# Kernel tuning notes

Hardware: AMD Instinct MI355X
Metric: run time of the kernel (lower is better)

The kernel has to match this reference:

```python
import jax, jax.numpy as jnp
import numpy as np

EPS = 1e-12  # torch F.normalize default eps


def l2_normalize_c(x):
    # F.normalize over channel dim (dim=1): x / max(||x||_2, eps)
    nrm = jnp.sqrt(jnp.sum(x * x, axis=1, keepdims=True))
    return x / jnp.maximum(nrm, EPS)


def resize_bilinear_ac(x, H, W):
    # bilinear, align_corners=True (matches torch F.interpolate)
    n, c, h, w = x.shape
    ys = jnp.linspace(0.0, h - 1.0, H)
    xs = jnp.linspace(0.0, w - 1.0, W)
    y0 = jnp.floor(ys).astype(jnp.int32)
    y1 = jnp.minimum(y0 + 1, h - 1)
    wy = (ys - y0.astype(ys.dtype))[:, None]          # [H,1]
    x0 = jnp.floor(xs).astype(jnp.int32)
    x1 = jnp.minimum(x0 + 1, w - 1)
    wx = xs - x0.astype(xs.dtype)                      # [W]
    rows = x[:, :, y0, :] * (1.0 - wy) + x[:, :, y1, :] * wy   # [n,c,H,w]
    return rows[:, :, :, x0] * (1.0 - wx) + rows[:, :, :, x1] * wx  # [n,c,H,W]


def unfold_3x3_d2(x):
    # nn.Unfold(kernel=3, dilation=2, padding=2, stride=1) viewed as [n,c,9,h,w]
    n, c, h, w = x.shape
    xp = jnp.pad(x, ((0, 0), (0, 0), (2, 2), (2, 2)))
    return jnp.stack(
        [xp[:, :, dy:dy + h, dx:dx + w] for dy in (0, 2, 4) for dx in (0, 2, 4)],
        axis=2,
    )  # [n,c,9,h,w], kernel index row-major (ky*3+kx) matching torch unfold


def setup_inputs() -> dict:
    key = jax.random.key(0)
    k1, k2, k3, k4, k5 = jax.random.split(key, 5)
    return {
        "c1": jax.random.normal(k1, (4, 256, 128, 128), dtype=jnp.float32),
        "c2": jax.random.normal(k2, (4, 512, 64, 64), dtype=jnp.float32),
        "out": jax.random.normal(k3, (4, 256, 64, 64), dtype=jnp.float32),
        "w_refine": jax.random.normal(k4, (32, 256), dtype=jnp.float32) * 0.05,
        "w_refine2": jax.random.normal(k5, (32, 512), dtype=jnp.float32) * 0.05,
    }


def reference(c1, c2, out, w_refine, w_refine2):
    n, _, h, w = c1.shape
    # 1x1 conv (no bias) + L2 normalize over channels
    q = l2_normalize_c(jnp.einsum("nchw,kc->nkhw", c1, w_refine))       # [n,32,h,w]
    c2u = resize_bilinear_ac(c2, h, w)
    kft = l2_normalize_c(jnp.einsum("nchw,kc->nkhw", c2u, w_refine2))    # [n,32,h,w]
    kpat = unfold_3x3_d2(kft)                                            # [n,32,9,h,w]
    energy = jnp.einsum("nchw,nckhw->nkhw", q, kpat)                     # [n,9,h,w]
    att = jax.nn.softmax(energy, axis=1)
    outu = resize_bilinear_ac(out, h, w)                                 # [n,C,h,w]
    vpat = unfold_3x3_d2(outu)                                           # [n,C,9,h,w]
    return jnp.einsum("nkhw,nckhw->nchw", att, vpat)
```

## Files before the change

kernel.cpp:

```cpp
#include <hip/hip_runtime.h>
#include <hip/hip_bf16.h>


typedef float f32x4 __attribute__((ext_vector_type(4)));
typedef float f32x2 __attribute__((ext_vector_type(2)));

#define SCL (63.0f / 127.0f)

__global__ __launch_bounds__(1024) void k_kfs(const float* __restrict__ c2,
                                              const float* __restrict__ wr2,
                                              float* __restrict__ kfs) {
    __shared__ float red[8 * 32 * 66];
    int b = blockIdx.x;
    int n = b >> 6;
    int pblk = (b & 63) * 64;
    int t = threadIdx.x;
    int lane = t & 63;
    int w = t >> 6;
    int cg = __builtin_amdgcn_readfirstlane(w & 7);
    int og = __builtin_amdgcn_readfirstlane(w >> 3);

    const float* src = c2 + ((size_t)n * 512 + cg * 64) * 4096 + pblk + lane;
    const float* wp  = wr2 + (og * 16) * 512 + cg * 64;

    float acc[16];
#pragma unroll
    for (int o = 0; o < 16; ++o) acc[o] = 0.f;
#pragma unroll 4
    for (int c = 0; c < 64; ++c) {
        float v = src[(size_t)c * 4096];
#pragma unroll
        for (int o = 0; o < 16; ++o)
            acc[o] = fmaf(v, wp[o * 512 + c], acc[o]);
    }
#pragma unroll
    for (int o = 0; o < 16; ++o)
        red[(cg * 32 + og * 16 + o) * 66 + lane] = acc[o];
    __syncthreads();

    if (t < 512) {
        int px = t & 63, seg = t >> 6;
        float v[4];
#pragma unroll
        for (int j = 0; j < 4; ++j) {
            float r = 0.f;
#pragma unroll
            for (int g = 0; g < 8; ++g) r += red[(g * 32 + seg * 4 + j) * 66 + px];
            v[j] = r;
        }
        f32x4 o4 = { v[0], v[1], v[2], v[3] };
        *(f32x4*)(kfs + ((size_t)n * 4096 + pblk + px) * 32 + seg * 4) = o4;
    }
}

__global__ __launch_bounds__(256) void k_upnorm(const float* __restrict__ kfs,
                                                float* __restrict__ kft) {
    int g = blockIdx.x * 256 + threadIdx.x;
    int p = g >> 2, qt = g & 3;
    int n = p >> 14;
    int rem = p & 16383;
    int y = rem >> 7, x = rem & 127;
    float syf = SCL * (float)y; int y0 = (int)syf; float fy = syf - (float)y0;
    int y1 = min(y0 + 1, 63);
    float sxf = SCL * (float)x; int x0 = (int)sxf; float fx = sxf - (float)x0;
    int x1 = min(x0 + 1, 63);
    size_t base = (size_t)n * 4096 * 32 + qt * 8;
    const f32x4* p00 = (const f32x4*)(kfs + base + ((size_t)(y0 * 64 + x0)) * 32);
    const f32x4* p01 = (const f32x4*)(kfs + base + ((size_t)(y0 * 64 + x1)) * 32);
    const f32x4* p10 = (const f32x4*)(kfs + base + ((size_t)(y1 * 64 + x0)) * 32);
    const f32x4* p11 = (const f32x4*)(kfs + base + ((size_t)(y1 * 64 + x1)) * 32);
    float w00 = (1.f-fy)*(1.f-fx), w01 = (1.f-fy)*fx, w10 = fy*(1.f-fx), w11 = fy*fx;
    float v[8]; float s = 0.f;
#pragma unroll
    for (int j = 0; j < 2; ++j) {
        f32x4 a = p00[j], b = p01[j], c = p10[j], d = p11[j];
#pragma unroll
        for (int tt = 0; tt < 4; ++tt) {
            float r = a[tt]*w00 + b[tt]*w01 + c[tt]*w10 + d[tt]*w11;
            v[4*j + tt] = r;
            s = fmaf(r, r, s);
        }
    }
    s += __shfl_xor(s, 1, 4);
    s += __shfl_xor(s, 2, 4);
    float inv = 1.0f / fmaxf(sqrtf(s), 1e-12f);
    f32x4* dst = (f32x4*)(kft + (size_t)p * 32 + qt * 8);
#pragma unroll
    for (int j = 0; j < 2; ++j) {
        f32x4 t = { v[4*j]*inv, v[4*j+1]*inv, v[4*j+2]*inv, v[4*j+3]*inv };
        dst[j] = t;
    }
}

__global__ __launch_bounds__(512) void k_fq3(const float* __restrict__ c1,
                                             const float* __restrict__ wr,
                                             const float* __restrict__ kft,
                                             float* __restrict__ wbuf) {
    __shared__ float smem[16640];
    const int WOFF = 4224;
    int b = blockIdx.x;
    int n = b >> 7;
    int y = b & 127;
    int pblk = y * 128;
    int t = threadIdx.x;
    int lane = t & 63;
    int w = t >> 6;
    int cg = __builtin_amdgcn_readfirstlane(w & 3);
    int og = __builtin_amdgcn_readfirstlane(w >> 2);

    {
        const float* src = c1 + ((size_t)n * 256 + cg * 64) * 16384 + pblk + lane * 2;
        const float* wp  = wr + (og * 16) * 256 + cg * 64;
        float acc0[16], acc1[16];
#pragma unroll
        for (int o = 0; o < 16; ++o) { acc0[o] = 0.f; acc1[o] = 0.f; }
        f32x2 n0 = *(const f32x2*)(src + (size_t)0 * 16384);
        f32x2 n1 = *(const f32x2*)(src + (size_t)1 * 16384);
        f32x2 n2 = *(const f32x2*)(src + (size_t)2 * 16384);
        f32x2 n3 = *(const f32x2*)(src + (size_t)3 * 16384);
#pragma unroll
        for (int cb = 0; cb < 16; ++cb) {
            f32x2 u0 = n0, u1 = n1, u2 = n2, u3 = n3;
            if (cb < 15) {
                const float* s2 = src + (size_t)(cb * 4 + 4) * 16384;
                n0 = *(const f32x2*)(s2 + (size_t)0 * 16384);
                n1 = *(const f32x2*)(s2 + (size_t)1 * 16384);
                n2 = *(const f32x2*)(s2 + (size_t)2 * 16384);
                n3 = *(const f32x2*)(s2 + (size_t)3 * 16384);
            }
#pragma unroll
            for (int o = 0; o < 16; ++o) {
                float w0 = wp[o * 256 + cb * 4 + 0];
                float w1 = wp[o * 256 + cb * 4 + 1];
                float w2 = wp[o * 256 + cb * 4 + 2];
                float w3 = wp[o * 256 + cb * 4 + 3];
                acc0[o] = fmaf(u0[0], w0, acc0[o]); acc1[o] = fmaf(u0[1], w0, acc1[o]);
                acc0[o] = fmaf(u1[0], w1, acc0[o]); acc1[o] = fmaf(u1[1], w1, acc1[o]);
                acc0[o] = fmaf(u2[0], w2, acc0[o]); acc1[o] = fmaf(u2[1], w2, acc1[o]);
                acc0[o] = fmaf(u3[0], w3, acc0[o]); acc1[o] = fmaf(u3[1], w3, acc1[o]);
            }
        }
#pragma unroll
        for (int o = 0; o < 16; ++o) {
            f32x2 pr = { acc0[o], acc1[o] };
            *(f32x2*)&smem[(cg * 32 + og * 16 + o) * 130 + lane * 2] = pr;
        }
    }
    __syncthreads();

    float v16[16];
    {
        int px = t & 127, half = (t >> 7) & 1;
        if (t < 256) {
#pragma unroll
            for (int o = 0; o < 16; ++o) {
                v16[o] = smem[(0 * 32 + half * 16 + o) * 130 + px]
                       + smem[(1 * 32 + half * 16 + o) * 130 + px]
                       + smem[(2 * 32 + half * 16 + o) * 130 + px]
                       + smem[(3 * 32 + half * 16 + o) * 130 + px];
            }
        }
    }
    __syncthreads();
    if (t < 256) {
        int px = t & 127, half = (t >> 7) & 1;
#pragma unroll
        for (int o = 0; o < 16; ++o) smem[px * 33 + half * 16 + o] = v16[o];
    }
    __syncthreads();

    {
        int px = t >> 2, qt = t & 3;
        int x = px;
        int ybase2 = min((int)(SCL * (float)max(y - 2, 0)), 60);
        int xbase2 = min((int)(SCL * (float)max(x - 2, 0)), 60);

        float qv[8];
#pragma unroll
        for (int j = 0; j < 8; ++j) qv[j] = smem[px * 33 + qt * 8 + j];
        float qs = 0.f;
#pragma unroll
        for (int j = 0; j < 8; ++j) qs = fmaf(qv[j], qv[j], qs);

        float d[9];
#pragma unroll
        for (int ky = 0; ky < 3; ++ky) {
            int ny = y + 2 * ky - 2;
            bool rowOK = (ny >= 0) && (ny < 128);
#pragma unroll
            for (int kx = 0; kx < 3; ++kx) {
                int nx = x + 2 * kx - 2;
                float acc = 0.f;
                if (rowOK && nx >= 0 && nx < 128) {
                    const f32x4* kp = (const f32x4*)(kft + ((size_t)n * 16384 + ny * 128 + nx) * 32 + qt * 8);
                    f32x4 a = kp[0], b2 = kp[1];
                    acc = fmaf(a[0],  qv[0], acc); acc = fmaf(a[1],  qv[1], acc);
                    acc = fmaf(a[2],  qv[2], acc); acc = fmaf(a[3],  qv[3], acc);
                    acc = fmaf(b2[0], qv[4], acc); acc = fmaf(b2[1], qv[5], acc);
                    acc = fmaf(b2[2], qv[6], acc); acc = fmaf(b2[3], qv[7], acc);
                }
                d[ky * 3 + kx] = acc;
            }
        }
        qs += __shfl_xor(qs, 1, 4); qs += __shfl_xor(qs, 2, 4);
#pragma unroll
        for (int k = 0; k < 9; ++k) {
            d[k] += __shfl_xor(d[k], 1, 4);
            d[k] += __shfl_xor(d[k], 2, 4);
        }
        float qinv = 1.0f / fmaxf(sqrtf(qs), 1e-12f);

        float e[9];
        float m = d[0] * qinv;
#pragma unroll
        for (int k = 0; k < 9; ++k) { e[k] = d[k] * qinv; if (k) m = fmaxf(m, e[k]); }
        float ssum = 0.f;
#pragma unroll
        for (int k = 0; k < 9; ++k) { e[k] = __expf(e[k] - m); ssum += e[k]; }
        float rinv = 1.0f / ssum;

        float* wp = smem + WOFF + px * 17;
#pragma unroll
        for (int i = 0; i < 16; ++i) wp[i] = 0.f;
#pragma unroll
        for (int ky = 0; ky < 3; ++ky) {
            int ny = y + 2 * ky - 2;
            if (ny < 0 || ny > 127) continue;
            float syf = SCL * (float)ny; int iy0 = (int)syf; float fy = syf - (float)iy0;
            int iy1 = min(iy0 + 1, 63);
            int r0 = (iy0 - ybase2) * 4, r1 = (iy1 - ybase2) * 4;
#pragma unroll
            for (int kx = 0; kx < 3; ++kx) {
                int nx = x + 2 * kx - 2;
                if (nx < 0 || nx > 127) continue;
                float sxf = SCL * (float)nx; int ix0 = (int)sxf; float fx = sxf - (float)ix0;
                int ix1 = min(ix0 + 1, 63);
                float a = e[ky * 3 + kx] * rinv;
                wp[r0 + (ix0 - xbase2)] += a * (1.f - fy) * (1.f - fx);
                wp[r0 + (ix1 - xbase2)] += a * (1.f - fy) * fx;
                wp[r1 + (ix0 - xbase2)] += a * fy * (1.f - fx);
                wp[r1 + (ix1 - xbase2)] += a * fy * fx;
            }
        }
    }
    __syncthreads();

    int sx = t & 127, i0 = t >> 7;
    int pg = n * 16384 + y * 128 + sx;
#pragma unroll
    for (int r = 0; r < 4; ++r) {
        int i = r * 4 + i0;
        wbuf[i * 65536 + pg] = smem[WOFF + sx * 17 + i];
    }
}

__global__ __launch_bounds__(256) void k_agg3(const float* __restrict__ wbuf,
                                              const float* __restrict__ outp,
                                              float* __restrict__ res) {
    __shared__ float wlds[128 * 17];
    int b = blockIdx.x;
    int cg = b & 3, y = (b >> 2) & 127, n = b >> 9;
    int t = threadIdx.x;
    int px2 = t & 63, cq = t >> 6;

    int ybase = min((int)(SCL * (float)max(y - 2, 0)), 60);
    int pix = n * 16384 + y * 128;

#pragma unroll
    for (int k = 0; k < 8; ++k) {
        int u = t + 256 * k;
        int i = u >> 7, xx = u & 127;
        wlds[xx * 17 + i] = wbuf[i * 65536 + pix + xx];
    }
    __syncthreads();

    int x0 = px2 * 2, x1 = x0 + 1;
    int xb0 = min((int)(SCL * (float)max(x0 - 2, 0)), 60);
    int xb1 = min((int)(SCL * (float)max(x1 - 2, 0)), 60);
    bool sh = (xb1 != xb0);
    int j4 = sh ? 4 : 3;
    float wA[16], wB[16];
#pragma unroll
    for (int i = 0; i < 16; ++i) {
        wA[i] = wlds[x0 * 17 + i];
        wB[i] = wlds[x1 * 17 + i];
    }

    const float* ob = outp + ((size_t)n * 256 + cg * 64 + cq * 16) * 4096 + ybase * 64 + xb0;
    float* rb = res + ((size_t)n * 256 + cg * 64 + cq * 16) * 16384 + y * 128 + x0;

#pragma unroll 2
    for (int i = 0; i < 16; ++i) {
        const float* tp = ob + (size_t)i * 4096;
        float a0 = 0.f, a1 = 0.f;
#pragma unroll
        for (int r = 0; r < 4; ++r) {
            float c0 = tp[r * 64 + 0];
            float c1 = tp[r * 64 + 1];
            float c2 = tp[r * 64 + 2];
            float c3 = tp[r * 64 + 3];
            float c4 = tp[r * 64 + j4];
            a0 = fmaf(wA[r*4+0], c0, a0);
            a0 = fmaf(wA[r*4+1], c1, a0);
            a0 = fmaf(wA[r*4+2], c2, a0);
            a0 = fmaf(wA[r*4+3], c3, a0);
            float s0 = sh ? c1 : c0;
            float s1 = sh ? c2 : c1;
            float s2 = sh ? c3 : c2;
            float s3 = sh ? c4 : c3;
            a1 = fmaf(wB[r*4+0], s0, a1);
            a1 = fmaf(wB[r*4+1], s1, a1);
            a1 = fmaf(wB[r*4+2], s2, a1);
            a1 = fmaf(wB[r*4+3], s3, a1);
        }
        f32x2 st = { a0, a1 };
        *(f32x2*)(rb + (size_t)i * 16384) = st;
    }
}

extern "C" void kernel_launch(void* const* d_in, const int* in_sizes, int n_in,
                              void* d_out, int out_size, void* d_ws, size_t ws_size,
                              hipStream_t stream) {
    const float* c1   = (const float*)d_in[0];
    const float* c2   = (const float*)d_in[1];
    const float* outp = (const float*)d_in[2];
    const float* wr   = (const float*)d_in[3];
    const float* wr2  = (const float*)d_in[4];
    float* res = (float*)d_out;

    float* kfs_ws = (float*)d_ws;
    float* kft_ws = (float*)((char*)d_ws + 2097152);
    float* w_ws   = (float*)((char*)d_ws + 2097152 + 8388608);

    hipLaunchKernelGGL(k_kfs,    dim3(256),  dim3(1024), 0, stream, c2, wr2, kfs_ws);
    hipLaunchKernelGGL(k_upnorm, dim3(1024), dim3(256),  0, stream, kfs_ws, kft_ws);
    hipLaunchKernelGGL(k_fq3,    dim3(512),  dim3(512),  0, stream, c1, wr, kft_ws, w_ws);
    hipLaunchKernelGGL(k_agg3,   dim3(2048), dim3(256),  0, stream, w_ws, outp, res);
}
```

Baseline: 79.73 us.

## Stage 4-row source tile in LDS with register double-buffered prefetch in aggregation

The final aggregation kernel now loads each channel's 4 source rows (4x64 floats) into shared memory with coalesced float4 loads, then reads the dilated 3x3 taps from LDS. Channels are handled in batches of 16, and the next batch is prefetched into registers while the current one is computed. This replaces scattered, overlapping per-thread global loads with one cooperative coalesced load per row, and removes redundant L1/L2 traffic. The cost is extra barriers and LDS use. Each thread also now computes 4 channels per batch instead of 16 strided channels.

Result: faster. 76.27 us (-4.3%).

```diff
diff --git a/kernel.cpp b/kernel.cpp
--- a/kernel.cpp
+++ b/kernel.cpp
@@ -254,14 +254,15 @@
     }
 }
 
-__global__ __launch_bounds__(256) void k_agg3(const float* __restrict__ wbuf,
+__global__ __launch_bounds__(256) void k_agg4(const float* __restrict__ wbuf,
                                               const float* __restrict__ outp,
                                               float* __restrict__ res) {
     __shared__ float wlds[128 * 17];
+    __shared__ float tile[16 * 260];
     int b = blockIdx.x;
     int cg = b & 3, y = (b >> 2) & 127, n = b >> 9;
     int t = threadIdx.x;
-    int px2 = t & 63, cq = t >> 6;
+    int px2 = t & 63, cq = t >> 6, seg = t & 63;
 
     int ybase = min((int)(SCL * (float)max(y - 2, 0)), 60);
     int pix = n * 16384 + y * 128;
@@ -278,7 +279,6 @@
     int xb0 = min((int)(SCL * (float)max(x0 - 2, 0)), 60);
     int xb1 = min((int)(SCL * (float)max(x1 - 2, 0)), 60);
     bool sh = (xb1 != xb0);
-    int j4 = sh ? 4 : 3;
     float wA[16], wB[16];
 #pragma unroll
     for (int i = 0; i < 16; ++i) {
@@ -286,35 +286,57 @@
         wB[i] = wlds[x1 * 17 + i];
     }
 
-    const float* ob = outp + ((size_t)n * 256 + cg * 64 + cq * 16) * 4096 + ybase * 64 + xb0;
-    float* rb = res + ((size_t)n * 256 + cg * 64 + cq * 16) * 16384 + y * 128 + x0;
-
-#pragma unroll 2
-    for (int i = 0; i < 16; ++i) {
-        const float* tp = ob + (size_t)i * 4096;
-        float a0 = 0.f, a1 = 0.f;
-#pragma unroll
-        for (int r = 0; r < 4; ++r) {
-            float c0 = tp[r * 64 + 0];
-            float c1 = tp[r * 64 + 1];
-            float c2 = tp[r * 64 + 2];
-            float c3 = tp[r * 64 + 3];
-            float c4 = tp[r * 64 + j4];
-            a0 = fmaf(wA[r*4+0], c0, a0);
-            a0 = fmaf(wA[r*4+1], c1, a0);
-            a0 = fmaf(wA[r*4+2], c2, a0);
-            a0 = fmaf(wA[r*4+3], c3, a0);
-            float s0 = sh ? c1 : c0;
-            float s1 = sh ? c2 : c1;
-            float s2 = sh ? c3 : c2;
-            float s3 = sh ? c4 : c3;
-            a1 = fmaf(wB[r*4+0], s0, a1);
-            a1 = fmaf(wB[r*4+1], s1, a1);
-            a1 = fmaf(wB[r*4+2], s2, a1);
-            a1 = fmaf(wB[r*4+3], s3, a1);
-        }
-        f32x2 st = { a0, a1 };
-        *(f32x2*)(rb + (size_t)i * 16384) = st;
+    const float* ob = outp + ((size_t)n * 256 + cg * 64) * 4096 + ybase * 64;
+    float* rb = res + ((size_t)n * 256 + cg * 64) * 16384 + y * 128 + x0;
+
+    f32x4 g0 = *(const f32x4*)(ob + (size_t)(cq + 0)  * 4096 + seg * 4);
+    f32x4 g1 = *(const f32x4*)(ob + (size_t)(cq + 4)  * 4096 + seg * 4);
+    f32x4 g2 = *(const f32x4*)(ob + (size_t)(cq + 8)  * 4096 + seg * 4);
+    f32x4 g3 = *(const f32x4*)(ob + (size_t)(cq + 12) * 4096 + seg * 4);
+
+#pragma unroll 1
+    for (int batch = 0; batch < 4; ++batch) {
+        __syncthreads();
+        *(f32x4*)&tile[(cq + 0)  * 260 + seg * 4] = g0;
+        *(f32x4*)&tile[(cq + 4)  * 260 + seg * 4] = g1;
+        *(f32x4*)&tile[(cq + 8)  * 260 + seg * 4] = g2;
+        *(f32x4*)&tile[(cq + 12) * 260 + seg * 4] = g3;
+        __syncthreads();
+        if (batch < 3) {
+            const float* s2 = ob + (size_t)(batch + 1) * 16 * 4096;
+            g0 = *(const f32x4*)(s2 + (size_t)(cq + 0)  * 4096 + seg * 4);
+            g1 = *(const f32x4*)(s2 + (size_t)(cq + 4)  * 4096 + seg * 4);
+            g2 = *(const f32x4*)(s2 + (size_t)(cq + 8)  * 4096 + seg * 4);
+            g3 = *(const f32x4*)(s2 + (size_t)(cq + 12) * 4096 + seg * 4);
+        }
+#pragma unroll
+        for (int cc = 0; cc < 4; ++cc) {
+            int c = cq * 4 + cc;
+            const float* tp = &tile[c * 260 + xb0];
+            float a0 = 0.f, a1 = 0.f;
+#pragma unroll
+            for (int r = 0; r < 4; ++r) {
+                float c0 = tp[r * 64 + 0];
+                float c1 = tp[r * 64 + 1];
+                float c2 = tp[r * 64 + 2];
+                float c3 = tp[r * 64 + 3];
+                float c4 = tp[r * 64 + 4];
+                a0 = fmaf(wA[r*4+0], c0, a0);
+                a0 = fmaf(wA[r*4+1], c1, a0);
+                a0 = fmaf(wA[r*4+2], c2, a0);
+                a0 = fmaf(wA[r*4+3], c3, a0);
+                float s0 = sh ? c1 : c0;
+                float s1 = sh ? c2 : c1;
+                float s2v = sh ? c3 : c2;
+                float s3 = sh ? c4 : c3;
+                a1 = fmaf(wB[r*4+0], s0, a1);
+                a1 = fmaf(wB[r*4+1], s1, a1);
+                a1 = fmaf(wB[r*4+2], s2v, a1);
+                a1 = fmaf(wB[r*4+3], s3, a1);
+            }
+            f32x2 st = { a0, a1 };
+            *(f32x2*)(rb + (size_t)(batch * 16 + c) * 16384) = st;
+        }
     }
 }
 
@@ -335,5 +357,5 @@
     hipLaunchKernelGGL(k_kfs,    dim3(256),  dim3(1024), 0, stream, c2, wr2, kfs_ws);
     hipLaunchKernelGGL(k_upnorm, dim3(1024), dim3(256),  0, stream, kfs_ws, kft_ws);
     hipLaunchKernelGGL(k_fq3,    dim3(512),  dim3(512),  0, stream, c1, wr, kft_ws, w_ws);
-    hipLaunchKernelGGL(k_agg3,   dim3(2048), dim3(256),  0, stream, w_ws, outp, res);
-}
+    hipLaunchKernelGGL(k_agg4,   dim3(2048), dim3(256),  0, stream, w_ws, outp, res);
+}
```
